# Kernel optimization log

Hardware: AMD Instinct MI355X
Metric: run time of the kernel (lower is better)

Reference implementation:

```python
import jax, jax.numpy as jnp
import numpy as np

B, T, NN, GP, D, H = 16, 12, 325, 64, 512, 8
HD = D // H
N_TOT = GP + NN  # 389


def setup_inputs() -> dict:
    key = jax.random.key(0)
    ks = jax.random.split(key, 16)
    def lin_w(k, fan_in, fan_out):
        return jax.random.normal(k, (fan_in, fan_out), jnp.float32) * np.float32(1.0 / np.sqrt(fan_in))
    d = {"X": jax.random.normal(ks[0], (B, T, N_TOT, D), jnp.float32)}
    i = 1
    for p in ("e", "d"):
        for w in ("q", "k", "v", "o"):
            d[f"{p}_w{w}"] = lin_w(ks[i], D, D); i += 1
            d[f"{p}_b{w}"] = jnp.zeros((D,), jnp.float32)
    d["ff_w1"] = lin_w(ks[i], D, 4 * D); i += 1
    d["ff_b1"] = jnp.zeros((4 * D,), jnp.float32)
    d["ff_w2"] = lin_w(ks[i], 4 * D, D); i += 1
    d["ff_b2"] = jnp.zeros((D,), jnp.float32)
    d["ln1_g"] = jnp.ones((D,), jnp.float32)
    d["ln1_b"] = jnp.zeros((D,), jnp.float32)
    d["ln2_g"] = jnp.ones((D,), jnp.float32)
    d["ln2_b"] = jnp.zeros((D,), jnp.float32)
    return d


def _mha(q, k, v, wq, bq, wk, bk, wv, bv, wo, bo):
    # torch split(head_dim,-1)+cat(0) == reshape last dim to (H, HD)
    Q = (q @ wq + bq).reshape(q.shape[:-1] + (H, HD))
    K = (k @ wk + bk).reshape(k.shape[:-1] + (H, HD))
    V = (v @ wv + bv).reshape(v.shape[:-1] + (H, HD))
    s = jnp.einsum('btqhd,btkhd->bthqk', Q, K) * np.float32(1.0 / np.sqrt(HD))
    a = jax.nn.softmax(s, axis=-1)  # dropout=0.0 -> identity
    o = jnp.einsum('bthqk,btkhd->btqhd', a, V).reshape(q.shape)
    return o @ wo + bo


def _ln(x, g, b):
    m = x.mean(-1, keepdims=True)
    v = x.var(-1, keepdims=True)
    return (x - m) * jax.lax.rsqrt(v + 1e-5) * g + b


def reference(X, e_wq, e_bq, e_wk, e_bk, e_wv, e_bv, e_wo, e_bo,
              d_wq, d_bq, d_wk, d_bk, d_wv, d_bv, d_wo, d_bo,
              ff_w1, ff_b1, ff_w2, ff_b2, ln1_g, ln1_b, ln2_g, ln2_b):
    glob = X[:, :, :GP, :]   # global patch queries
    patch = X[:, :, GP:, :]  # last num_nodes tokens (== x[:,:,-patch_len:])
    # eattn: global queries attend to node tokens
    t = _mha(glob, patch, patch, e_wq, e_bq, e_wk, e_bk, e_wv, e_bv, e_wo, e_bo)
    # in-place write x[:,:,:global_patch] = t -> K/V for dattn is [t, patch]
    x_kv = jnp.concatenate([t, patch], axis=2)
    # dattn: node queries attend to full (updated) sequence
    out = _mha(patch, x_kv, x_kv, d_wq, d_bq, d_wk, d_bk, d_wv, d_bv, d_wo, d_bo)
    out = _ln(patch + out, ln1_g, ln1_b)  # residual is original node tokens
    ff = jax.nn.relu(out @ ff_w1 + ff_b1) @ ff_w2 + ff_b2
    out = _ln(out + ff, ln2_g, ln2_b)
    return jnp.concatenate([t, out], axis=2)
```

## Files before the change

kernel.cpp:

```cpp
#include <hip/hip_runtime.h>

typedef unsigned short u16;
typedef __attribute__((ext_vector_type(4))) float f32x4;
typedef __attribute__((ext_vector_type(8))) __bf16 bf16x8;
typedef __attribute__((ext_vector_type(4))) unsigned short u16x4;
typedef __attribute__((ext_vector_type(8))) unsigned short u16x8;

#define DEV static __device__ __forceinline__


DEV u16 f2b(float f) {
  union { float f; unsigned u; } c; c.f = f;
  return (u16)((c.u + 0x7FFFu + ((c.u >> 16) & 1u)) >> 16);
}

DEV void async_cp16(void* lds, const void* g) {
  __builtin_amdgcn_global_load_lds((__attribute__((address_space(1))) void*)g,
                                   (__attribute__((address_space(3))) void*)lds,
                                   16, 0, 0);
}

__global__ __launch_bounds__(256) void transpose_w(const float* __restrict__ W,
                                                   u16* __restrict__ Wt,
                                                   int K, int N) {
  __shared__ float t[32][33];
  const int n0 = blockIdx.x * 32, k0 = blockIdx.y * 32;
  const int tx = threadIdx.x, ty = threadIdx.y;
  for (int i = ty; i < 32; i += 8) t[i][tx] = W[(size_t)(k0 + i) * N + n0 + tx];
  __syncthreads();
  for (int i = ty; i < 32; i += 8)
    Wt[(size_t)(n0 + i) * K + k0 + tx] = f2b(t[tx][i]);
}

__global__ __launch_bounds__(256) void convert_x(const float* __restrict__ X,
                                                 u16* __restrict__ Xg,
                                                 u16* __restrict__ Xp) {
  const size_t i = ((size_t)blockIdx.x * 256 + threadIdx.x) * 4;
  const f32x4 v = *(const f32x4*)(X + i);
  const size_t row = i >> 9;
  const int col = (int)(i & 511);
  const int bt = (int)(row / 389), n = (int)(row - (size_t)bt * 389);
  u16x4 w;
#pragma unroll
  for (int u = 0; u < 4; u++) w[u] = f2b(v[u]);
  u16* dst = (n < 64) ? (Xg + (((size_t)bt * 64 + n) << 9) + col)
                      : (Xp + (((size_t)bt * 325 + (n - 64)) << 9) + col);
  *(u16x4*)dst = w;
}

template <int MODE>
__global__ __launch_bounds__(256) void gemm_bt(
    const u16* __restrict__ A, const u16* __restrict__ Bt,
    const float* __restrict__ bias, float* outF, u16* outB,
    int M, int N, int K, int rows_per, int row_ofs, int vt_stride) {
  __shared__ u16 As[128 * 64];
  __shared__ u16 Bs[128 * 64];
  const int tid = threadIdx.x;
  const int lane = tid & 63, wid = tid >> 6;
  const int l4 = lane >> 4, l16 = lane & 15;
  const int m0 = blockIdx.x * 128, n0 = blockIdx.y * 128;
  const int wr = (wid >> 1) * 64, wc = (wid & 1) * 64;

  const int srow = lane >> 3;
  const int scol = 8 * ((lane & 7) ^ srow);
  const u16* gA = A + (size_t)(m0 + wid * 32 + srow) * K + scol;
  const u16* gB = Bt + (size_t)(n0 + wid * 32 + srow) * K + scol;

  f32x4 acc[4][4] = {};

  for (int kk = 0; kk < K; kk += 64) {
    if (kk) __syncthreads();
#pragma unroll
    for (int c = 0; c < 4; c++) {
      async_cp16(As + (wid * 32 + c * 8) * 64, gA + (size_t)(c * 8) * K + kk);
      async_cp16(Bs + (wid * 32 + c * 8) * 64, gB + (size_t)(c * 8) * K + kk);
    }
    __syncthreads();
#pragma unroll
    for (int h = 0; h < 2; h++) {
      const int sw = (((h * 64 + l4 * 16) ^ ((l16 & 7) << 4)) >> 1);
      bf16x8 af[4], bfr[4];
#pragma unroll
      for (int i = 0; i < 4; i++)
        af[i] = *(const bf16x8*)(As + (wr + i * 16 + l16) * 64 + sw);
#pragma unroll
      for (int j = 0; j < 4; j++)
        bfr[j] = *(const bf16x8*)(Bs + (wc + j * 16 + l16) * 64 + sw);
#pragma unroll
      for (int i = 0; i < 4; i++)
#pragma unroll
        for (int j = 0; j < 4; j++)
          acc[i][j] = __builtin_amdgcn_mfma_f32_16x16x32_bf16(af[i], bfr[j],
                                                              acc[i][j], 0, 0, 0);
    }
  }

#pragma unroll
  for (int j = 0; j < 4; j++) {
    const int col = n0 + wc + j * 16 + l16;
    const float bv = bias[col];
#pragma unroll
    for (int i = 0; i < 4; i++) {
#pragma unroll
      for (int r = 0; r < 4; r++) {
        const int row = m0 + wr + i * 16 + l4 * 4 + r;
        if (row >= M) continue;
        const float v = acc[i][j][r] + bv;
        if constexpr (MODE == 0) {
          outB[(size_t)row * N + col] = f2b(v);
        } else if constexpr (MODE == 1) {
          const int bt = row / rows_per, rr = row - bt * rows_per;
          outB[((size_t)bt * 389 + row_ofs + rr) * 512 + col] = f2b(v);
        } else if constexpr (MODE == 2) {
          const int bt = row >> 6, rr = row & 63;
          outF[((size_t)bt * 389 + rr) * 512 + col] = v;
          outB[(size_t)row * 512 + col] = f2b(v);
        } else if constexpr (MODE == 3) {
          outF[(size_t)row * N + col] = v;
        } else if constexpr (MODE == 4) {
          outB[(size_t)row * N + col] = f2b(v > 0.f ? v : 0.f);
        } else if constexpr (MODE == 5) {
          outF[(size_t)row * N + col] += v;
        } else {
          const int bt = row / rows_per, rr = row - bt * rows_per;
          const int h = col >> 6, d = col & 63;
          outB[(((size_t)bt * 8 + h) * 64 + d) * (size_t)vt_stride +
               (row_ofs + rr)] = f2b(v);
        }
      }
    }
  }
}

template <int MQ, int NK, int NKP>
__global__ __launch_bounds__(256, 4) void attn_fused(const u16* __restrict__ Q,
                                                     const u16* __restrict__ Kb,
                                                     const u16* __restrict__ Vt,
                                                     u16* __restrict__ O) {
  constexpr int NCH = NKP / 32;
  constexpr int QC = (MQ + 63) / 64;
  __shared__ __align__(16) u16 Pl[4][16 * 40];
  const int tid = threadIdx.x, lane = tid & 63, wid = tid >> 6;
  const int l4 = lane >> 4, l16 = lane & 15;
  const int bt = blockIdx.x >> 3, h = blockIdx.x & 7;
  u16* pw = &Pl[wid][0];
  const u16* vbase = Vt + ((size_t)bt * 8 + h) * 64 * NKP;

  for (int qc = 0; qc < QC; ++qc) {
    const int q0 = qc * 64 + wid * 16;
    if (q0 >= MQ) continue;
    const u16* qp = Q + ((size_t)bt * MQ + q0 + l16) * 512 + h * 64 + l4 * 8;
    const bf16x8 aq0 = *(const bf16x8*)qp;
    const bf16x8 aq1 = *(const bf16x8*)(qp + 32);

    f32x4 m, sum, o[4];
#pragma unroll
    for (int r = 0; r < 4; r++) { m[r] = -1e30f; sum[r] = 0.f; }
#pragma unroll
    for (int j = 0; j < 4; j++) o[j] = (f32x4){0.f, 0.f, 0.f, 0.f};

    for (int ch = 0; ch < NCH; ++ch) {
      const int k0 = ch * 32;
      const u16* kp0 = Kb + ((size_t)bt * NK + k0 + l16) * 512 + h * 64 + l4 * 8;
      const u16* kp1 = kp0 + (size_t)16 * 512;
      f32x4 sA = {0.f, 0.f, 0.f, 0.f}, sB = {0.f, 0.f, 0.f, 0.f};
      sA = __builtin_amdgcn_mfma_f32_16x16x32_bf16(aq0, *(const bf16x8*)kp0, sA, 0, 0, 0);
      sA = __builtin_amdgcn_mfma_f32_16x16x32_bf16(aq1, *(const bf16x8*)(kp0 + 32), sA, 0, 0, 0);
      sB = __builtin_amdgcn_mfma_f32_16x16x32_bf16(aq0, *(const bf16x8*)kp1, sB, 0, 0, 0);
      sB = __builtin_amdgcn_mfma_f32_16x16x32_bf16(aq1, *(const bf16x8*)(kp1 + 32), sB, 0, 0, 0);
      const bool vA = (k0 + l16) < NK, vB = (k0 + 16 + l16) < NK;
      f32x4 cm;
#pragma unroll
      for (int r = 0; r < 4; r++) {
        sA[r] = vA ? sA[r] * 0.125f : -1e30f;
        sB[r] = vB ? sB[r] * 0.125f : -1e30f;
        cm[r] = fmaxf(sA[r], sB[r]);
      }
#pragma unroll
      for (int mk = 1; mk < 16; mk <<= 1)
#pragma unroll
        for (int r = 0; r < 4; r++) cm[r] = fmaxf(cm[r], __shfl_xor(cm[r], mk));
      float fr[4];
#pragma unroll
      for (int r = 0; r < 4; r++) {
        const float mn = fmaxf(m[r], cm[r]);
        fr[r] = __expf(m[r] - mn);
        m[r] = mn;
        sA[r] = __expf(sA[r] - mn);
        sB[r] = __expf(sB[r] - mn);
        sum[r] = sum[r] * fr[r] + sA[r] + sB[r];
      }
#pragma unroll
      for (int j = 0; j < 4; j++)
#pragma unroll
        for (int r = 0; r < 4; r++) o[j][r] *= fr[r];
#pragma unroll
      for (int r = 0; r < 4; r++) {
        pw[(l4 * 4 + r) * 40 + l16] = f2b(sA[r]);
        pw[(l4 * 4 + r) * 40 + 16 + l16] = f2b(sB[r]);
      }
      asm volatile("s_waitcnt lgkmcnt(0)" ::: "memory");
      const bf16x8 ap = *(const bf16x8*)(pw + l16 * 40 + l4 * 8);
      __builtin_amdgcn_s_setprio(1);
#pragma unroll
      for (int j = 0; j < 4; j++) {
        const bf16x8 bv = *(const bf16x8*)(vbase + (size_t)(j * 16 + l16) * NKP +
                                           k0 + l4 * 8);
        o[j] = __builtin_amdgcn_mfma_f32_16x16x32_bf16(ap, bv, o[j], 0, 0, 0);
      }
      __builtin_amdgcn_s_setprio(0);
    }
#pragma unroll
    for (int mk = 1; mk < 16; mk <<= 1)
#pragma unroll
      for (int r = 0; r < 4; r++) sum[r] += __shfl_xor(sum[r], mk);
    f32x4 inv;
#pragma unroll
    for (int r = 0; r < 4; r++) inv[r] = 1.f / sum[r];
#pragma unroll
    for (int j = 0; j < 4; j++)
#pragma unroll
      for (int r = 0; r < 4; r++) {
        const int qr = q0 + l4 * 4 + r;
        if (qr < MQ)
          O[((size_t)bt * MQ + qr) * 512 + h * 64 + j * 16 + l16] =
              f2b(o[j][r] * inv[r]);
      }
  }
}

__global__ __launch_bounds__(256) void ln_res(const float* X, const float* add,
                                              const float* g, const float* b,
                                              float* y, u16* yb) {
  const int p = blockIdx.x * 4 + (threadIdx.x >> 6);
  const int lane = threadIdx.x & 63;
  const int bt = p / 325, n = p - bt * 325;
  const float* xr = X + ((size_t)bt * 389 + 64 + n) * 512 + lane * 8;
  const float* ar = add + (size_t)p * 512 + lane * 8;
  float vv[8];
  {
    const f32x4 a0 = *(const f32x4*)xr, a1 = *(const f32x4*)(xr + 4);
    const f32x4 b0 = *(const f32x4*)ar, b1 = *(const f32x4*)(ar + 4);
#pragma unroll
    for (int u = 0; u < 4; u++) {
      vv[u] = a0[u] + b0[u];
      vv[u + 4] = a1[u] + b1[u];
    }
  }
  float s1 = 0.f, s2 = 0.f;
#pragma unroll
  for (int u = 0; u < 8; u++) {
    s1 += vv[u];
    s2 += vv[u] * vv[u];
  }
  for (int m = 1; m < 64; m <<= 1) {
    s1 += __shfl_xor(s1, m);
    s2 += __shfl_xor(s2, m);
  }
  const float mean = s1 * (1.f / 512.f);
  const float inv = rsqrtf(s2 * (1.f / 512.f) - mean * mean + 1e-5f);
  const int c0 = lane * 8;
  f32x4 o0, o1;
  u16x8 ob;
#pragma unroll
  for (int u = 0; u < 8; u++) {
    const float o = (vv[u] - mean) * inv * g[c0 + u] + b[c0 + u];
    if (u < 4) o0[u] = o; else o1[u - 4] = o;
    ob[u] = f2b(o);
  }
  *(f32x4*)(y + (size_t)p * 512 + c0) = o0;
  *(f32x4*)(y + (size_t)p * 512 + c0 + 4) = o1;
  *(u16x8*)(yb + (size_t)p * 512 + c0) = ob;
}

__global__ __launch_bounds__(256) void ln_out(const float* y, const float* g,
                                              const float* b, float* out) {
  const int p = blockIdx.x * 4 + (threadIdx.x >> 6);
  const int lane = threadIdx.x & 63;
  const int bt = p / 325, n = p - bt * 325;
  const float* yr = y + (size_t)p * 512 + lane * 8;
  float vv[8];
  {
    const f32x4 a0 = *(const f32x4*)yr, a1 = *(const f32x4*)(yr + 4);
#pragma unroll
    for (int u = 0; u < 4; u++) {
      vv[u] = a0[u];
      vv[u + 4] = a1[u];
    }
  }
  float s1 = 0.f, s2 = 0.f;
#pragma unroll
  for (int u = 0; u < 8; u++) {
    s1 += vv[u];
    s2 += vv[u] * vv[u];
  }
  for (int m = 1; m < 64; m <<= 1) {
    s1 += __shfl_xor(s1, m);
    s2 += __shfl_xor(s2, m);
  }
  const float mean = s1 * (1.f / 512.f);
  const float inv = rsqrtf(s2 * (1.f / 512.f) - mean * mean + 1e-5f);
  const int c0 = lane * 8;
  f32x4 o0, o1;
#pragma unroll
  for (int u = 0; u < 8; u++) {
    const float o = (vv[u] - mean) * inv * g[c0 + u] + b[c0 + u];
    if (u < 4) o0[u] = o; else o1[u - 4] = o;
  }
  float* orow = out + ((size_t)bt * 389 + 64 + n) * 512 + c0;
  *(f32x4*)(orow) = o0;
  *(f32x4*)(orow + 4) = o1;
}

extern "C" void kernel_launch(void* const* d_in, const int* in_sizes, int n_in,
                              void* d_out, int out_size, void* d_ws,
                              size_t ws_size, hipStream_t stream) {
  (void)in_sizes; (void)n_in; (void)out_size; (void)ws_size;
  const float* X = (const float*)d_in[0];
  const float* W[8] = {(const float*)d_in[1],  (const float*)d_in[3],
                       (const float*)d_in[5],  (const float*)d_in[7],
                       (const float*)d_in[9],  (const float*)d_in[11],
                       (const float*)d_in[13], (const float*)d_in[15]};
  const float* Bv[8] = {(const float*)d_in[2],  (const float*)d_in[4],
                        (const float*)d_in[6],  (const float*)d_in[8],
                        (const float*)d_in[10], (const float*)d_in[12],
                        (const float*)d_in[14], (const float*)d_in[16]};
  const float* ff_w1 = (const float*)d_in[17];
  const float* ff_b1 = (const float*)d_in[18];
  const float* ff_w2 = (const float*)d_in[19];
  const float* ff_b2 = (const float*)d_in[20];
  const float* ln1_g = (const float*)d_in[21];
  const float* ln1_b = (const float*)d_in[22];
  const float* ln2_g = (const float*)d_in[23];
  const float* ln2_b = (const float*)d_in[24];
  float* out = (float*)d_out;
  char* ws = (char*)d_ws;

  constexpr size_t MG = 12288, MP = 62400, MKV = 74688, PADR = 128;
  const size_t szQe = (MG + PADR) * 1024;
  const size_t szKe = (MP + PADR) * 1024;
  const size_t szVte = (size_t)192 * 8 * 64 * 352 * 2;
  const size_t szKd = (MKV + PADR) * 1024;
  const size_t szVtd = (size_t)192 * 8 * 64 * 416 * 2;
  const size_t szY = MP * 2048;
  const size_t szH = (size_t)(15616 + PADR) * 2048 * 2;

  size_t off = 0;
  const size_t o_wt = off; off += (size_t)4194304 * 2;
  const size_t o_AD = off; off += szY;
  size_t b1 = szQe + szKe + szVte;
  size_t b2 = szKe + szKd + szVtd;
  size_t b3 = szKe + szH;
  size_t szB = b1 > b2 ? b1 : b2; if (b3 > szB) szB = b3;
  const size_t o_B = off; off += szB;
  const size_t o_C = off; off += szKe;

  u16* wt = (u16*)(ws + o_wt);
  u16* Xg = (u16*)(ws + o_AD);
  u16* Xp = (u16*)(ws + o_AD + szQe);
  float* y = (float*)(ws + o_AD);
  u16* Qe = (u16*)(ws + o_B);
  u16* Ke = (u16*)(ws + o_B + szQe);
  u16* Vte = (u16*)(ws + o_B + szQe + szKe);
  u16* Qd = (u16*)(ws + o_B);
  u16* Kd = (u16*)(ws + o_B + szKe);
  u16* Vtd = (u16*)(ws + o_B + szKe + szKd);
  u16* yb = (u16*)(ws + o_B);
  u16* hb = (u16*)(ws + o_B + szKe);
  u16* attn_e = (u16*)(ws + o_C);
  u16* tb = (u16*)(ws + o_C + szQe);
  u16* attn_d = (u16*)(ws + o_C);

  u16* wt_p[8];
  for (int i = 0; i < 8; i++) wt_p[i] = wt + (size_t)i * 262144;
  u16* ff1t = wt + (size_t)8 * 262144;
  u16* ff2t = ff1t + (size_t)1048576;

  dim3 tblk(32, 8);
  for (int i = 0; i < 8; i++)
    transpose_w<<<dim3(16, 16), tblk, 0, stream>>>(W[i], wt_p[i], 512, 512);
  transpose_w<<<dim3(64, 16), tblk, 0, stream>>>(ff_w1, ff1t, 512, 2048);
  transpose_w<<<dim3(16, 64), tblk, 0, stream>>>(ff_w2, ff2t, 2048, 512);

  convert_x<<<37344, 256, 0, stream>>>(X, Xg, Xp);

  gemm_bt<0><<<dim3(96, 4), 256, 0, stream>>>(Xg, wt_p[0], Bv[0], nullptr, Qe,
                                              (int)MG, 512, 512, 0, 0, 0);
  gemm_bt<0><<<dim3(488, 4), 256, 0, stream>>>(Xp, wt_p[1], Bv[1], nullptr, Ke,
                                               (int)MP, 512, 512, 0, 0, 0);
  gemm_bt<6><<<dim3(488, 4), 256, 0, stream>>>(Xp, wt_p[2], Bv[2], nullptr, Vte,
                                               (int)MP, 512, 512, 325, 0, 352);
  attn_fused<64, 325, 352><<<1536, 256, 0, stream>>>(Qe, Ke, Vte, attn_e);
  gemm_bt<2><<<dim3(96, 4), 256, 0, stream>>>(attn_e, wt_p[3], Bv[3], out, tb,
                                              (int)MG, 512, 512, 0, 0, 0);

  gemm_bt<0><<<dim3(488, 4), 256, 0, stream>>>(Xp, wt_p[4], Bv[4], nullptr, Qd,
                                               (int)MP, 512, 512, 0, 0, 0);
  gemm_bt<1><<<dim3(96, 4), 256, 0, stream>>>(tb, wt_p[5], Bv[5], nullptr, Kd,
                                              (int)MG, 512, 512, 64, 0, 0);
  gemm_bt<1><<<dim3(488, 4), 256, 0, stream>>>(Xp, wt_p[5], Bv[5], nullptr, Kd,
                                               (int)MP, 512, 512, 325, 64, 0);
  gemm_bt<6><<<dim3(96, 4), 256, 0, stream>>>(tb, wt_p[6], Bv[6], nullptr, Vtd,
                                              (int)MG, 512, 512, 64, 0, 416);
  gemm_bt<6><<<dim3(488, 4), 256, 0, stream>>>(Xp, wt_p[6], Bv[6], nullptr, Vtd,
                                               (int)MP, 512, 512, 325, 64, 416);
  attn_fused<325, 389, 416><<<1536, 256, 0, stream>>>(Qd, Kd, Vtd, attn_d);
  gemm_bt<3><<<dim3(488, 4), 256, 0, stream>>>(attn_d, wt_p[7], Bv[7], y,
                                               nullptr, (int)MP, 512, 512, 0, 0,
                                               0);

  ln_res<<<15600, 256, 0, stream>>>(X, y, ln1_g, ln1_b, y, yb);

  const int c0s[4] = {0, 15616, 31232, 46848};
  const int mcs[4] = {15616, 15616, 15616, 15552};
  for (int c = 0; c < 4; c++) {
    gemm_bt<4><<<dim3((mcs[c] + 127) / 128, 16), 256, 0, stream>>>(
        yb + (size_t)c0s[c] * 512, ff1t, ff_b1, nullptr, hb, mcs[c], 2048, 512,
        0, 0, 0);
    gemm_bt<5><<<dim3((mcs[c] + 127) / 128, 4), 256, 0, stream>>>(
        hb, ff2t, ff_b2, y + (size_t)c0s[c] * 512, nullptr, mcs[c], 512, 2048,
        0, 0, 0);
  }
  ln_out<<<15600, 256, 0, stream>>>(y, ln2_g, ln2_b, out);
}
```

Measured before the change: 2.150 ms.

## Pad node rows to 328, widen attention chunks, stage V-transpose stores via LDS

Node tokens are padded from 325 to 328 rows per (b,t), so every GEMM runs over aligned row counts and the FFN chunks split evenly. The GEMM grid is reordered so blockIdx.x walks the N tiles, letting adjacent blocks share A rows. The transposed-V epilogue now goes through shared memory and writes 8-wide vectors instead of scattered 2-byte stores. Attention processes 64-key chunks, skips the rescale when no row max grows, and in the decoder attention one wave handles two 16-query tiles so K and V loads are reused. The cost is extra padded work, more registers in attention, and a fully reshuffled workspace layout.

After: 2.048 ms. -4.8%, faster.

```diff
diff --git a/kernel.cpp b/kernel.cpp
--- a/kernel.cpp
+++ b/kernel.cpp
@@ -7,6 +7,7 @@
 typedef __attribute__((ext_vector_type(8))) unsigned short u16x8;
 
 #define DEV static __device__ __forceinline__
+#define MFMA_B16 __builtin_amdgcn_mfma_f32_16x16x32_bf16
 
 
 DEV u16 f2b(float f) {
@@ -44,7 +45,7 @@
 #pragma unroll
   for (int u = 0; u < 4; u++) w[u] = f2b(v[u]);
   u16* dst = (n < 64) ? (Xg + (((size_t)bt * 64 + n) << 9) + col)
-                      : (Xp + (((size_t)bt * 325 + (n - 64)) << 9) + col);
+                      : (Xp + (((size_t)bt * 328 + (n - 64)) << 9) + col);
   *(u16x4*)dst = w;
 }
 
@@ -52,13 +53,14 @@
 __global__ __launch_bounds__(256) void gemm_bt(
     const u16* __restrict__ A, const u16* __restrict__ Bt,
     const float* __restrict__ bias, float* outF, u16* outB,
-    int M, int N, int K, int rows_per, int row_ofs, int vt_stride) {
-  __shared__ u16 As[128 * 64];
-  __shared__ u16 Bs[128 * 64];
+    int M, int N, int K, int rows_per, int row_ofs, int aux) {
+  __shared__ u16 SH[2][128 * 64];
+  u16* As = &SH[0][0];
+  u16* Bs = &SH[1][0];
   const int tid = threadIdx.x;
   const int lane = tid & 63, wid = tid >> 6;
   const int l4 = lane >> 4, l16 = lane & 15;
-  const int m0 = blockIdx.x * 128, n0 = blockIdx.y * 128;
+  const int n0 = blockIdx.x * 128, m0 = blockIdx.y * 128;
   const int wr = (wid >> 1) * 64, wc = (wid & 1) * 64;
 
   const int srow = lane >> 3;
@@ -77,8 +79,8 @@
     }
     __syncthreads();
 #pragma unroll
-    for (int h = 0; h < 2; h++) {
-      const int sw = (((h * 64 + l4 * 16) ^ ((l16 & 7) << 4)) >> 1);
+    for (int hh = 0; hh < 2; hh++) {
+      const int sw = (((hh * 64 + l4 * 16) ^ ((l16 & 7) << 4)) >> 1);
       bf16x8 af[4], bfr[4];
 #pragma unroll
       for (int i = 0; i < 4; i++)
@@ -90,173 +92,258 @@
       for (int i = 0; i < 4; i++)
 #pragma unroll
         for (int j = 0; j < 4; j++)
-          acc[i][j] = __builtin_amdgcn_mfma_f32_16x16x32_bf16(af[i], bfr[j],
-                                                              acc[i][j], 0, 0, 0);
-    }
-  }
-
-#pragma unroll
-  for (int j = 0; j < 4; j++) {
-    const int col = n0 + wc + j * 16 + l16;
-    const float bv = bias[col];
-#pragma unroll
-    for (int i = 0; i < 4; i++) {
-#pragma unroll
-      for (int r = 0; r < 4; r++) {
-        const int row = m0 + wr + i * 16 + l4 * 4 + r;
-        if (row >= M) continue;
-        const float v = acc[i][j][r] + bv;
-        if constexpr (MODE == 0) {
-          outB[(size_t)row * N + col] = f2b(v);
-        } else if constexpr (MODE == 1) {
-          const int bt = row / rows_per, rr = row - bt * rows_per;
-          outB[((size_t)bt * 389 + row_ofs + rr) * 512 + col] = f2b(v);
-        } else if constexpr (MODE == 2) {
-          const int bt = row >> 6, rr = row & 63;
-          outF[((size_t)bt * 389 + rr) * 512 + col] = v;
-          outB[(size_t)row * 512 + col] = f2b(v);
-        } else if constexpr (MODE == 3) {
-          outF[(size_t)row * N + col] = v;
-        } else if constexpr (MODE == 4) {
-          outB[(size_t)row * N + col] = f2b(v > 0.f ? v : 0.f);
-        } else if constexpr (MODE == 5) {
-          outF[(size_t)row * N + col] += v;
-        } else {
-          const int bt = row / rows_per, rr = row - bt * rows_per;
-          const int h = col >> 6, d = col & 63;
-          outB[(((size_t)bt * 8 + h) * 64 + d) * (size_t)vt_stride +
-               (row_ofs + rr)] = f2b(v);
-        }
-      }
-    }
-  }
-}
-
-template <int MQ, int NK, int NKP>
-__global__ __launch_bounds__(256, 4) void attn_fused(const u16* __restrict__ Q,
-                                                     const u16* __restrict__ Kb,
-                                                     const u16* __restrict__ Vt,
-                                                     u16* __restrict__ O) {
-  constexpr int NCH = NKP / 32;
-  constexpr int QC = (MQ + 63) / 64;
-  __shared__ __align__(16) u16 Pl[4][16 * 40];
+          acc[i][j] = MFMA_B16(af[i], bfr[j], acc[i][j], 0, 0, 0);
+    }
+  }
+
+  if constexpr (MODE == 6) {
+    __syncthreads();
+    u16* cs = &SH[0][0];
+#pragma unroll
+    for (int j = 0; j < 4; j++) {
+      const float bv = bias[n0 + wc + j * 16 + l16];
+#pragma unroll
+      for (int i = 0; i < 4; i++)
+#pragma unroll
+        for (int r = 0; r < 4; r++)
+          cs[(wr + i * 16 + l4 * 4 + r) * 128 + wc + j * 16 + l16] =
+              f2b(acc[i][j][r] + bv);
+    }
+    __syncthreads();
+    const int c = tid & 127;
+    const int kvh = (tid >> 7) * 64;
+    const int gh = (n0 + c) >> 6, gd = (n0 + c) & 63;
+#pragma unroll
+    for (int g = 0; g < 8; g++) {
+      const int row0 = m0 + kvh + g * 8;
+      if (row0 >= M) break;
+      const int bt0 = row0 / rows_per;
+      const int rr = row0 - bt0 * rows_per;
+      u16x8 w;
+#pragma unroll
+      for (int e = 0; e < 8; e++) w[e] = cs[(kvh + g * 8 + e) * 128 + c];
+      *(u16x8*)(outB + (((size_t)bt0 * 8 + gh) * 64 + gd) * (size_t)aux +
+                row_ofs + rr) = w;
+    }
+  } else {
+#pragma unroll
+    for (int j = 0; j < 4; j++) {
+      const int col = n0 + wc + j * 16 + l16;
+      const float bv = bias[col];
+#pragma unroll
+      for (int i = 0; i < 4; i++) {
+#pragma unroll
+        for (int r = 0; r < 4; r++) {
+          const int row = m0 + wr + i * 16 + l4 * 4 + r;
+          if (row >= M) continue;
+          const float v = acc[i][j][r] + bv;
+          if constexpr (MODE == 0) {
+            outB[(size_t)row * N + col] = f2b(v);
+          } else if constexpr (MODE == 1) {
+            const int bt = row / rows_per, rr = row - bt * rows_per;
+            if (rr < aux)
+              outB[((size_t)bt * 389 + row_ofs + rr) * 512 + col] = f2b(v);
+          } else if constexpr (MODE == 2) {
+            const int bt = row >> 6, rr = row & 63;
+            outF[((size_t)bt * 389 + rr) * 512 + col] = v;
+            outB[(size_t)row * 512 + col] = f2b(v);
+          } else if constexpr (MODE == 3) {
+            outF[(size_t)row * N + col] = v;
+          } else if constexpr (MODE == 4) {
+            outB[(size_t)row * N + col] = f2b(v > 0.f ? v : 0.f);
+          } else {
+            outF[(size_t)row * N + col] += v;
+          }
+        }
+      }
+    }
+  }
+}
+
+template <int QS, int MQ, int KS, int NK, int NKP, bool T2>
+__global__ __launch_bounds__(256) void attn_fused(
+    const u16* __restrict__ Q, const u16* __restrict__ Kb,
+    const u16* __restrict__ Vt, u16* __restrict__ O) {
+  constexpr int NCH = NKP / 64;
+  constexpr int QTW = T2 ? 128 : 64;
+  constexpr int QP = (MQ + QTW - 1) / QTW;
+  constexpr int PSTR = 72;
+  __shared__ __align__(16) u16 Pl[4][2][16 * PSTR];
   const int tid = threadIdx.x, lane = tid & 63, wid = tid >> 6;
   const int l4 = lane >> 4, l16 = lane & 15;
   const int bt = blockIdx.x >> 3, h = blockIdx.x & 7;
-  u16* pw = &Pl[wid][0];
-  const u16* vbase = Vt + ((size_t)bt * 8 + h) * 64 * NKP;
-
-  for (int qc = 0; qc < QC; ++qc) {
-    const int q0 = qc * 64 + wid * 16;
-    if (q0 >= MQ) continue;
-    const u16* qp = Q + ((size_t)bt * MQ + q0 + l16) * 512 + h * 64 + l4 * 8;
-    const bf16x8 aq0 = *(const bf16x8*)qp;
-    const bf16x8 aq1 = *(const bf16x8*)(qp + 32);
-
-    f32x4 m, sum, o[4];
-#pragma unroll
-    for (int r = 0; r < 4; r++) { m[r] = -1e30f; sum[r] = 0.f; }
-#pragma unroll
-    for (int j = 0; j < 4; j++) o[j] = (f32x4){0.f, 0.f, 0.f, 0.f};
+  u16* pw0 = &Pl[wid][0][0];
+  u16* pw1 = &Pl[wid][1][0];
+  const u16* vb = Vt + ((size_t)bt * 8 + h) * (size_t)(64 * NKP);
+  const u16* qb = Q + (size_t)bt * QS * 512 + h * 64;
+  const u16* kb = Kb + (size_t)bt * KS * 512 + h * 64;
+
+  for (int qp = 0; qp < QP; ++qp) {
+    const int q0 = qp * QTW + wid * 16;
+    const bool bL = T2 && (q0 + 64 < MQ);
+    const u16* qpA = qb + (size_t)(q0 + l16) * 512 + l4 * 8;
+    const bf16x8 aq0A = *(const bf16x8*)qpA;
+    const bf16x8 aq1A = *(const bf16x8*)(qpA + 32);
+    bf16x8 aq0B, aq1B;
+    if (bL) {
+      aq0B = *(const bf16x8*)(qpA + 32768);
+      aq1B = *(const bf16x8*)(qpA + 32768 + 32);
+    }
+
+    f32x4 m0v, m1v, sum0, sum1, o0[4], o1[4];
+#pragma unroll
+    for (int r = 0; r < 4; r++) {
+      m0v[r] = -1e30f; m1v[r] = -1e30f; sum0[r] = 0.f; sum1[r] = 0.f;
+    }
+#pragma unroll
+    for (int j = 0; j < 4; j++) {
+      o0[j] = (f32x4){0.f, 0.f, 0.f, 0.f};
+      o1[j] = (f32x4){0.f, 0.f, 0.f, 0.f};
+    }
 
     for (int ch = 0; ch < NCH; ++ch) {
-      const int k0 = ch * 32;
-      const u16* kp0 = Kb + ((size_t)bt * NK + k0 + l16) * 512 + h * 64 + l4 * 8;
-      const u16* kp1 = kp0 + (size_t)16 * 512;
-      f32x4 sA = {0.f, 0.f, 0.f, 0.f}, sB = {0.f, 0.f, 0.f, 0.f};
-      sA = __builtin_amdgcn_mfma_f32_16x16x32_bf16(aq0, *(const bf16x8*)kp0, sA, 0, 0, 0);
-      sA = __builtin_amdgcn_mfma_f32_16x16x32_bf16(aq1, *(const bf16x8*)(kp0 + 32), sA, 0, 0, 0);
-      sB = __builtin_amdgcn_mfma_f32_16x16x32_bf16(aq0, *(const bf16x8*)kp1, sB, 0, 0, 0);
-      sB = __builtin_amdgcn_mfma_f32_16x16x32_bf16(aq1, *(const bf16x8*)(kp1 + 32), sB, 0, 0, 0);
-      const bool vA = (k0 + l16) < NK, vB = (k0 + 16 + l16) < NK;
-      f32x4 cm;
+      const int k0 = ch * 64;
+      f32x4 sc0[4], sc1[4];
+#pragma unroll
+      for (int s = 0; s < 4; s++) {
+        const u16* kp = kb + (size_t)(k0 + s * 16 + l16) * 512 + l4 * 8;
+        const bf16x8 kf0 = *(const bf16x8*)kp;
+        const bf16x8 kf1 = *(const bf16x8*)(kp + 32);
+        f32x4 a = (f32x4){0.f, 0.f, 0.f, 0.f};
+        a = MFMA_B16(aq0A, kf0, a, 0, 0, 0);
+        a = MFMA_B16(aq1A, kf1, a, 0, 0, 0);
+        sc0[s] = a;
+        if (bL) {
+          f32x4 bacc = (f32x4){0.f, 0.f, 0.f, 0.f};
+          bacc = MFMA_B16(aq0B, kf0, bacc, 0, 0, 0);
+          bacc = MFMA_B16(aq1B, kf1, bacc, 0, 0, 0);
+          sc1[s] = bacc;
+        }
+      }
+#pragma unroll
+      for (int s = 0; s < 4; s++) {
+        const bool vld = (k0 + s * 16 + l16) < NK;
+#pragma unroll
+        for (int r = 0; r < 4; r++) {
+          sc0[s][r] = vld ? sc0[s][r] * 0.125f : -1e30f;
+          if (bL) sc1[s][r] = vld ? sc1[s][r] * 0.125f : -1e30f;
+        }
+      }
+      f32x4 c0, c1;
 #pragma unroll
       for (int r = 0; r < 4; r++) {
-        sA[r] = vA ? sA[r] * 0.125f : -1e30f;
-        sB[r] = vB ? sB[r] * 0.125f : -1e30f;
-        cm[r] = fmaxf(sA[r], sB[r]);
+        c0[r] = fmaxf(fmaxf(sc0[0][r], sc0[1][r]), fmaxf(sc0[2][r], sc0[3][r]));
+        if (bL)
+          c1[r] = fmaxf(fmaxf(sc1[0][r], sc1[1][r]), fmaxf(sc1[2][r], sc1[3][r]));
       }
 #pragma unroll
       for (int mk = 1; mk < 16; mk <<= 1)
 #pragma unroll
-        for (int r = 0; r < 4; r++) cm[r] = fmaxf(cm[r], __shfl_xor(cm[r], mk));
-      float fr[4];
+        for (int r = 0; r < 4; r++) {
+          c0[r] = fmaxf(c0[r], __shfl_xor(c0[r], mk));
+          if (bL) c1[r] = fmaxf(c1[r], __shfl_xor(c1[r], mk));
+        }
+      float g = c0[0] - m0v[0];
+#pragma unroll
+      for (int r = 1; r < 4; r++) g = fmaxf(g, c0[r] - m0v[r]);
+      if (bL)
+#pragma unroll
+        for (int r = 0; r < 4; r++) g = fmaxf(g, c1[r] - m1v[r]);
+      if (__any(g > 0.f)) {
+#pragma unroll
+        for (int r = 0; r < 4; r++) {
+          float mn = fmaxf(m0v[r], c0[r]);
+          float f = __expf(m0v[r] - mn);
+          m0v[r] = mn; sum0[r] *= f;
+#pragma unroll
+          for (int j = 0; j < 4; j++) o0[j][r] *= f;
+          if (bL) {
+            mn = fmaxf(m1v[r], c1[r]); f = __expf(m1v[r] - mn);
+            m1v[r] = mn; sum1[r] *= f;
+#pragma unroll
+            for (int j = 0; j < 4; j++) o1[j][r] *= f;
+          }
+        }
+      }
+#pragma unroll
+      for (int s = 0; s < 4; s++)
+#pragma unroll
+        for (int r = 0; r < 4; r++) {
+          const float e0 = __expf(sc0[s][r] - m0v[r]);
+          sum0[r] += e0;
+          pw0[(l4 * 4 + r) * PSTR + s * 16 + l16] = f2b(e0);
+          if (bL) {
+            const float e1 = __expf(sc1[s][r] - m1v[r]);
+            sum1[r] += e1;
+            pw1[(l4 * 4 + r) * PSTR + s * 16 + l16] = f2b(e1);
+          }
+        }
+      asm volatile("s_waitcnt lgkmcnt(0)" ::: "memory");
+      const bf16x8 apA0 = *(const bf16x8*)(pw0 + l16 * PSTR + l4 * 8);
+      const bf16x8 apA1 = *(const bf16x8*)(pw0 + l16 * PSTR + 32 + l4 * 8);
+      bf16x8 apB0, apB1;
+      if (bL) {
+        apB0 = *(const bf16x8*)(pw1 + l16 * PSTR + l4 * 8);
+        apB1 = *(const bf16x8*)(pw1 + l16 * PSTR + 32 + l4 * 8);
+      }
+      __builtin_amdgcn_s_setprio(1);
+#pragma unroll
+      for (int j = 0; j < 4; j++) {
+        const u16* vp = vb + (size_t)(j * 16 + l16) * NKP + k0 + l4 * 8;
+        const bf16x8 v0 = *(const bf16x8*)vp;
+        const bf16x8 v1 = *(const bf16x8*)(vp + 32);
+        o0[j] = MFMA_B16(apA0, v0, o0[j], 0, 0, 0);
+        o0[j] = MFMA_B16(apA1, v1, o0[j], 0, 0, 0);
+        if (bL) {
+          o1[j] = MFMA_B16(apB0, v0, o1[j], 0, 0, 0);
+          o1[j] = MFMA_B16(apB1, v1, o1[j], 0, 0, 0);
+        }
+      }
+      __builtin_amdgcn_s_setprio(0);
+    }
+#pragma unroll
+    for (int mk = 1; mk < 16; mk <<= 1)
 #pragma unroll
       for (int r = 0; r < 4; r++) {
-        const float mn = fmaxf(m[r], cm[r]);
-        fr[r] = __expf(m[r] - mn);
-        m[r] = mn;
-        sA[r] = __expf(sA[r] - mn);
-        sB[r] = __expf(sB[r] - mn);
-        sum[r] = sum[r] * fr[r] + sA[r] + sB[r];
-      }
-#pragma unroll
-      for (int j = 0; j < 4; j++)
-#pragma unroll
-        for (int r = 0; r < 4; r++) o[j][r] *= fr[r];
-#pragma unroll
-      for (int r = 0; r < 4; r++) {
-        pw[(l4 * 4 + r) * 40 + l16] = f2b(sA[r]);
-        pw[(l4 * 4 + r) * 40 + 16 + l16] = f2b(sB[r]);
-      }
-      asm volatile("s_waitcnt lgkmcnt(0)" ::: "memory");
-      const bf16x8 ap = *(const bf16x8*)(pw + l16 * 40 + l4 * 8);
-      __builtin_amdgcn_s_setprio(1);
-#pragma unroll
-      for (int j = 0; j < 4; j++) {
-        const bf16x8 bv = *(const bf16x8*)(vbase + (size_t)(j * 16 + l16) * NKP +
-                                           k0 + l4 * 8);
-        o[j] = __builtin_amdgcn_mfma_f32_16x16x32_bf16(ap, bv, o[j], 0, 0, 0);
-      }
-      __builtin_amdgcn_s_setprio(0);
-    }
-#pragma unroll
-    for (int mk = 1; mk < 16; mk <<= 1)
-#pragma unroll
-      for (int r = 0; r < 4; r++) sum[r] += __shfl_xor(sum[r], mk);
-    f32x4 inv;
-#pragma unroll
-    for (int r = 0; r < 4; r++) inv[r] = 1.f / sum[r];
+        sum0[r] += __shfl_xor(sum0[r], mk);
+        if (bL) sum1[r] += __shfl_xor(sum1[r], mk);
+      }
 #pragma unroll
     for (int j = 0; j < 4; j++)
 #pragma unroll
       for (int r = 0; r < 4; r++) {
         const int qr = q0 + l4 * 4 + r;
         if (qr < MQ)
-          O[((size_t)bt * MQ + qr) * 512 + h * 64 + j * 16 + l16] =
-              f2b(o[j][r] * inv[r]);
-      }
-  }
-}
-
-__global__ __launch_bounds__(256) void ln_res(const float* X, const float* add,
+          O[((size_t)bt * QS + qr) * 512 + h * 64 + j * 16 + l16] =
+              f2b(o0[j][r] / sum0[r]);
+        if (bL && qr + 64 < MQ)
+          O[((size_t)bt * QS + qr + 64) * 512 + h * 64 + j * 16 + l16] =
+              f2b(o1[j][r] / sum1[r]);
+      }
+  }
+}
+
+__global__ __launch_bounds__(256) void ln_res(const float* __restrict__ X,
+                                              float* __restrict__ y,
                                               const float* g, const float* b,
-                                              float* y, u16* yb) {
+                                              u16* __restrict__ yb) {
   const int p = blockIdx.x * 4 + (threadIdx.x >> 6);
   const int lane = threadIdx.x & 63;
   const int bt = p / 325, n = p - bt * 325;
+  const size_t yrow = ((size_t)bt * 328 + n) * 512;
   const float* xr = X + ((size_t)bt * 389 + 64 + n) * 512 + lane * 8;
-  const float* ar = add + (size_t)p * 512 + lane * 8;
+  const float* ar = y + yrow + lane * 8;
   float vv[8];
   {
     const f32x4 a0 = *(const f32x4*)xr, a1 = *(const f32x4*)(xr + 4);
     const f32x4 b0 = *(const f32x4*)ar, b1 = *(const f32x4*)(ar + 4);
 #pragma unroll
-    for (int u = 0; u < 4; u++) {
-      vv[u] = a0[u] + b0[u];
-      vv[u + 4] = a1[u] + b1[u];
-    }
+    for (int u = 0; u < 4; u++) { vv[u] = a0[u] + b0[u]; vv[u + 4] = a1[u] + b1[u]; }
   }
   float s1 = 0.f, s2 = 0.f;
 #pragma unroll
-  for (int u = 0; u < 8; u++) {
-    s1 += vv[u];
-    s2 += vv[u] * vv[u];
-  }
-  for (int m = 1; m < 64; m <<= 1) {
-    s1 += __shfl_xor(s1, m);
-    s2 += __shfl_xor(s2, m);
-  }
+  for (int u = 0; u < 8; u++) { s1 += vv[u]; s2 += vv[u] * vv[u]; }
+  for (int m = 1; m < 64; m <<= 1) { s1 += __shfl_xor(s1, m); s2 += __shfl_xor(s2, m); }
   const float mean = s1 * (1.f / 512.f);
   const float inv = rsqrtf(s2 * (1.f / 512.f) - mean * mean + 1e-5f);
   const int c0 = lane * 8;
@@ -268,36 +355,28 @@
     if (u < 4) o0[u] = o; else o1[u - 4] = o;
     ob[u] = f2b(o);
   }
-  *(f32x4*)(y + (size_t)p * 512 + c0) = o0;
-  *(f32x4*)(y + (size_t)p * 512 + c0 + 4) = o1;
-  *(u16x8*)(yb + (size_t)p * 512 + c0) = ob;
-}
-
-__global__ __launch_bounds__(256) void ln_out(const float* y, const float* g,
-                                              const float* b, float* out) {
+  *(f32x4*)(y + yrow + c0) = o0;
+  *(f32x4*)(y + yrow + c0 + 4) = o1;
+  *(u16x8*)(yb + yrow + c0) = ob;
+}
+
+__global__ __launch_bounds__(256) void ln_out(const float* __restrict__ y,
+                                              const float* g, const float* b,
+                                              float* __restrict__ out) {
   const int p = blockIdx.x * 4 + (threadIdx.x >> 6);
   const int lane = threadIdx.x & 63;
   const int bt = p / 325, n = p - bt * 325;
-  const float* yr = y + (size_t)p * 512 + lane * 8;
+  const float* yr = y + ((size_t)bt * 328 + n) * 512 + lane * 8;
   float vv[8];
   {
     const f32x4 a0 = *(const f32x4*)yr, a1 = *(const f32x4*)(yr + 4);
 #pragma unroll
-    for (int u = 0; u < 4; u++) {
-      vv[u] = a0[u];
-      vv[u + 4] = a1[u];
-    }
+    for (int u = 0; u < 4; u++) { vv[u] = a0[u]; vv[u + 4] = a1[u]; }
   }
   float s1 = 0.f, s2 = 0.f;
 #pragma unroll
-  for (int u = 0; u < 8; u++) {
-    s1 += vv[u];
-    s2 += vv[u] * vv[u];
-  }
-  for (int m = 1; m < 64; m <<= 1) {
-    s1 += __shfl_xor(s1, m);
-    s2 += __shfl_xor(s2, m);
-  }
+  for (int u = 0; u < 8; u++) { s1 += vv[u]; s2 += vv[u] * vv[u]; }
+  for (int m = 1; m < 64; m <<= 1) { s1 += __shfl_xor(s1, m); s2 += __shfl_xor(s2, m); }
   const float mean = s1 * (1.f / 512.f);
   const float inv = rsqrtf(s2 * (1.f / 512.f) - mean * mean + 1e-5f);
   const int c0 = lane * 8;
@@ -336,40 +415,35 @@
   float* out = (float*)d_out;
   char* ws = (char*)d_ws;
 
-  constexpr size_t MG = 12288, MP = 62400, MKV = 74688, PADR = 128;
-  const size_t szQe = (MG + PADR) * 1024;
-  const size_t szKe = (MP + PADR) * 1024;
-  const size_t szVte = (size_t)192 * 8 * 64 * 352 * 2;
-  const size_t szKd = (MKV + PADR) * 1024;
-  const size_t szVtd = (size_t)192 * 8 * 64 * 416 * 2;
-  const size_t szY = MP * 2048;
-  const size_t szH = (size_t)(15616 + PADR) * 2048 * 2;
-
-  size_t off = 0;
-  const size_t o_wt = off; off += (size_t)4194304 * 2;
-  const size_t o_AD = off; off += szY;
-  size_t b1 = szQe + szKe + szVte;
-  size_t b2 = szKe + szKd + szVtd;
-  size_t b3 = szKe + szH;
-  size_t szB = b1 > b2 ? b1 : b2; if (b3 > szB) szB = b3;
-  const size_t o_B = off; off += szB;
-  const size_t o_C = off; off += szKe;
-
-  u16* wt = (u16*)(ws + o_wt);
-  u16* Xg = (u16*)(ws + o_AD);
-  u16* Xp = (u16*)(ws + o_AD + szQe);
-  float* y = (float*)(ws + o_AD);
-  u16* Qe = (u16*)(ws + o_B);
-  u16* Ke = (u16*)(ws + o_B + szQe);
-  u16* Vte = (u16*)(ws + o_B + szQe + szKe);
-  u16* Qd = (u16*)(ws + o_B);
-  u16* Kd = (u16*)(ws + o_B + szKe);
-  u16* Vtd = (u16*)(ws + o_B + szKe + szKd);
-  u16* yb = (u16*)(ws + o_B);
-  u16* hb = (u16*)(ws + o_B + szKe);
-  u16* attn_e = (u16*)(ws + o_C);
-  u16* tb = (u16*)(ws + o_C + szQe);
-  u16* attn_d = (u16*)(ws + o_C);
+  constexpr size_t szW   = 8388608;
+  constexpr size_t szXp  = (size_t)(62976 + 128) * 1024;
+  constexpr size_t szQe  = (size_t)(12288 + 128) * 1024;
+  constexpr size_t szKe  = szXp;
+  constexpr size_t szVte = (size_t)192 * 8 * 64 * 384 * 2;
+  constexpr size_t szKd  = (size_t)(74688 + 128) * 1024;
+  constexpr size_t szVtd = (size_t)192 * 8 * 64 * 448 * 2;
+  constexpr size_t o1 = szW;
+  constexpr size_t o2 = o1 + szXp;
+  constexpr size_t o3 = o2 + szQe;
+  constexpr size_t o4 = o3 + szQe;
+  constexpr size_t o5 = o4 + szQe + szKe + szVte;
+  constexpr size_t o6 = o5 + szVtd;
+
+  u16* wt     = (u16*)(ws);
+  u16* Xp     = (u16*)(ws + o1);
+  u16* yb     = (u16*)(ws + o1);
+  u16* Xg     = (u16*)(ws + o2);
+  u16* attn_e = (u16*)(ws + o2);
+  u16* tb     = (u16*)(ws + o3);
+  u16* Qe     = (u16*)(ws + o4);
+  u16* Ke     = (u16*)(ws + o4 + szQe);
+  u16* Vte    = (u16*)(ws + o4 + szQe + szKe);
+  u16* Qd     = (u16*)(ws + o4);
+  u16* Kd     = (u16*)(ws + o4 + szXp);
+  float* y    = (float*)(ws + o4);
+  u16* Vtd    = (u16*)(ws + o5);
+  u16* hb     = (u16*)(ws + o5);
+  u16* attn_d = (u16*)(ws + o6);
 
   u16* wt_p[8];
   for (int i = 0; i < 8; i++) wt_p[i] = wt + (size_t)i * 262144;
@@ -384,42 +458,40 @@
 
   convert_x<<<37344, 256, 0, stream>>>(X, Xg, Xp);
 
-  gemm_bt<0><<<dim3(96, 4), 256, 0, stream>>>(Xg, wt_p[0], Bv[0], nullptr, Qe,
-                                              (int)MG, 512, 512, 0, 0, 0);
-  gemm_bt<0><<<dim3(488, 4), 256, 0, stream>>>(Xp, wt_p[1], Bv[1], nullptr, Ke,
-                                               (int)MP, 512, 512, 0, 0, 0);
-  gemm_bt<6><<<dim3(488, 4), 256, 0, stream>>>(Xp, wt_p[2], Bv[2], nullptr, Vte,
-                                               (int)MP, 512, 512, 325, 0, 352);
-  attn_fused<64, 325, 352><<<1536, 256, 0, stream>>>(Qe, Ke, Vte, attn_e);
-  gemm_bt<2><<<dim3(96, 4), 256, 0, stream>>>(attn_e, wt_p[3], Bv[3], out, tb,
-                                              (int)MG, 512, 512, 0, 0, 0);
-
-  gemm_bt<0><<<dim3(488, 4), 256, 0, stream>>>(Xp, wt_p[4], Bv[4], nullptr, Qd,
-                                               (int)MP, 512, 512, 0, 0, 0);
-  gemm_bt<1><<<dim3(96, 4), 256, 0, stream>>>(tb, wt_p[5], Bv[5], nullptr, Kd,
-                                              (int)MG, 512, 512, 64, 0, 0);
-  gemm_bt<1><<<dim3(488, 4), 256, 0, stream>>>(Xp, wt_p[5], Bv[5], nullptr, Kd,
-                                               (int)MP, 512, 512, 325, 64, 0);
-  gemm_bt<6><<<dim3(96, 4), 256, 0, stream>>>(tb, wt_p[6], Bv[6], nullptr, Vtd,
-                                              (int)MG, 512, 512, 64, 0, 416);
-  gemm_bt<6><<<dim3(488, 4), 256, 0, stream>>>(Xp, wt_p[6], Bv[6], nullptr, Vtd,
-                                               (int)MP, 512, 512, 325, 64, 416);
-  attn_fused<325, 389, 416><<<1536, 256, 0, stream>>>(Qd, Kd, Vtd, attn_d);
-  gemm_bt<3><<<dim3(488, 4), 256, 0, stream>>>(attn_d, wt_p[7], Bv[7], y,
-                                               nullptr, (int)MP, 512, 512, 0, 0,
-                                               0);
-
-  ln_res<<<15600, 256, 0, stream>>>(X, y, ln1_g, ln1_b, y, yb);
-
-  const int c0s[4] = {0, 15616, 31232, 46848};
-  const int mcs[4] = {15616, 15616, 15616, 15552};
+  gemm_bt<0><<<dim3(4, 96), 256, 0, stream>>>(Xg, wt_p[0], Bv[0], nullptr, Qe,
+                                              12288, 512, 512, 0, 0, 0);
+  gemm_bt<0><<<dim3(4, 492), 256, 0, stream>>>(Xp, wt_p[1], Bv[1], nullptr, Ke,
+                                               62976, 512, 512, 0, 0, 0);
+  gemm_bt<6><<<dim3(4, 492), 256, 0, stream>>>(Xp, wt_p[2], Bv[2], nullptr, Vte,
+                                               62976, 512, 512, 328, 0, 384);
+  attn_fused<64, 64, 328, 325, 384, false><<<1536, 256, 0, stream>>>(
+      Qe, Ke, Vte, attn_e);
+  gemm_bt<2><<<dim3(4, 96), 256, 0, stream>>>(attn_e, wt_p[3], Bv[3], out, tb,
+                                              12288, 512, 512, 0, 0, 0);
+
+  gemm_bt<0><<<dim3(4, 492), 256, 0, stream>>>(Xp, wt_p[4], Bv[4], nullptr, Qd,
+                                               62976, 512, 512, 0, 0, 0);
+  gemm_bt<1><<<dim3(4, 96), 256, 0, stream>>>(tb, wt_p[5], Bv[5], nullptr, Kd,
+                                              12288, 512, 512, 64, 0, 64);
+  gemm_bt<1><<<dim3(4, 492), 256, 0, stream>>>(Xp, wt_p[5], Bv[5], nullptr, Kd,
+                                               62976, 512, 512, 328, 64, 325);
+  gemm_bt<6><<<dim3(4, 96), 256, 0, stream>>>(tb, wt_p[6], Bv[6], nullptr, Vtd,
+                                              12288, 512, 512, 64, 0, 448);
+  gemm_bt<6><<<dim3(4, 492), 256, 0, stream>>>(Xp, wt_p[6], Bv[6], nullptr, Vtd,
+                                               62976, 512, 512, 328, 64, 448);
+  attn_fused<328, 325, 389, 389, 448, true><<<1536, 256, 0, stream>>>(
+      Qd, Kd, Vtd, attn_d);
+  gemm_bt<3><<<dim3(4, 492), 256, 0, stream>>>(attn_d, wt_p[7], Bv[7], y,
+                                               nullptr, 62976, 512, 512, 0, 0, 0);
+
+  ln_res<<<15600, 256, 0, stream>>>(X, y, ln1_g, ln1_b, yb);
+
   for (int c = 0; c < 4; c++) {
-    gemm_bt<4><<<dim3((mcs[c] + 127) / 128, 16), 256, 0, stream>>>(
-        yb + (size_t)c0s[c] * 512, ff1t, ff_b1, nullptr, hb, mcs[c], 2048, 512,
-        0, 0, 0);
-    gemm_bt<5><<<dim3((mcs[c] + 127) / 128, 4), 256, 0, stream>>>(
-        hb, ff2t, ff_b2, y + (size_t)c0s[c] * 512, nullptr, mcs[c], 512, 2048,
-        0, 0, 0);
+    const size_t ro = (size_t)c * 15744;
+    gemm_bt<4><<<dim3(16, 123), 256, 0, stream>>>(
+        yb + ro * 512, ff1t, ff_b1, nullptr, hb, 15744, 2048, 512, 0, 0, 0);
+    gemm_bt<5><<<dim3(4, 123), 256, 0, stream>>>(
+        hb, ff2t, ff_b2, y + ro * 512, nullptr, 15744, 512, 2048, 0, 0, 0);
   }
   ln_out<<<15600, 256, 0, stream>>>(y, ln2_g, ln2_b, out);
 }
```
